# Kernel tuning notes

Measured on AMD Instinct MI355X. Metric: run time of the kernel, lower is better.

Reference implementation:

```python
import jax, jax.numpy as jnp
import numpy as np

H = 1024
B, S = 8, 2048
EPS = 1e-5


def _layernorm(x, w, b):
    m = jnp.mean(x, axis=-1, keepdims=True)
    v = jnp.mean((x - m) ** 2, axis=-1, keepdims=True)
    return (x - m) * jax.lax.rsqrt(v + EPS) * w + b


def setup_inputs() -> dict:
    key = jax.random.key(0)
    ks = jax.random.split(key, 10)
    x = jax.random.normal(ks[0], (B, S, H), dtype=jnp.float32)
    # LayerNorm params (torch default init: weight=1, bias=0)
    qn_w = jnp.ones((H,), jnp.float32)
    qn_b = jnp.zeros((H,), jnp.float32)
    kvn_w = jnp.ones((H,), jnp.float32)
    kvn_b = jnp.zeros((H,), jnp.float32)
    # q_prime/k_prime/v_prime ~ U(-0.5, 0.5)
    q_prime = jax.random.uniform(ks[1], (1, H), jnp.float32) - 0.5
    k_prime = jax.random.uniform(ks[2], (1, H), jnp.float32) - 0.5
    v_prime = jax.random.uniform(ks[3], (1, H), jnp.float32) - 0.5
    # Linear params, torch-style fan_in init
    lim = 1.0 / np.sqrt(H)
    qW = jax.random.uniform(ks[4], (H, H), jnp.float32, -lim, lim)
    qb = jax.random.uniform(ks[5], (H,), jnp.float32, -lim, lim)
    v1W = jax.random.uniform(ks[6], (H, H), jnp.float32, -lim, lim)
    v1b = jax.random.uniform(ks[7], (H,), jnp.float32, -lim, lim)
    v2W = jax.random.uniform(ks[8], (H, H), jnp.float32, -lim, lim)
    v2b = jax.random.uniform(ks[9], (H,), jnp.float32, -lim, lim)
    return {"x": x, "qn_w": qn_w, "qn_b": qn_b, "kvn_w": kvn_w, "kvn_b": kvn_b,
            "q_prime": q_prime, "k_prime": k_prime, "v_prime": v_prime,
            "qW": qW, "qb": qb, "v1W": v1W, "v1b": v1b, "v2W": v2W, "v2b": v2b}


def reference(x, qn_w, qn_b, kvn_w, kvn_b, q_prime, k_prime, v_prime,
              qW, qb, v1W, v1b, v2W, v2b):
    divisor = jnp.sqrt(jnp.float32(x.shape[-1]))
    xqn = _layernorm(x, qn_w, qn_b)            # [B,S,H]
    xkvn = _layernorm(x, kvn_w, kvn_b)         # [B,S,H]
    kr = xkvn * jax.nn.sigmoid(k_prime)        # [B,S,H]
    qr = (xqn @ qW.T + qb) * jax.nn.sigmoid(q_prime)  # [B,S,H]
    vp = jax.nn.sigmoid(v_prime)               # [1,H]
    gate = jax.nn.sigmoid(vp @ v1W.T + v1b) * jnp.tanh(vp @ v2W.T + v2b)  # [1,H]
    vr = xkvn * gate                           # [B,S,H]
    scores = jnp.einsum('bsh,bth->bst', qr, kr) / divisor  # [B,S,S]
    b, s, t = scores.shape
    # global softmax over flattened seq x seq matrix
    attn = jax.nn.softmax(scores.reshape(b, s * t), axis=-1).reshape(b, s, t)
    attended = jnp.einsum('bst,bth->bsh', attn, vr)
    return attended + xqn
```

## Files before the change

kernel.cpp:

```cpp
#include <hip/hip_runtime.h>
#include <stdint.h>


#define DEVI __device__ __forceinline__

typedef __bf16 bf16x8 __attribute__((ext_vector_type(8)));
typedef float  f32x4  __attribute__((ext_vector_type(4)));

typedef __attribute__((address_space(3))) uint32_t lds_u32_t;
typedef __attribute__((address_space(1))) uint32_t glb_u32_t;

DEVI uint16_t f2bf(float f) {
  union { float f; uint32_t u; } v; v.f = f;
  uint32_t r = (v.u + 0x7fffu + ((v.u >> 16) & 1u)) >> 16;
  return (uint16_t)r;
}
DEVI float bf2f(uint16_t b) {
  union { uint32_t u; float f; } v; v.u = ((uint32_t)b) << 16;
  return v.f;
}
DEVI float sigm(float x) { return 1.0f / (1.0f + __expf(-x)); }

DEVI void gl_lds16(const void* g, const void* lds_base) {
  __builtin_amdgcn_global_load_lds((glb_u32_t*)(uintptr_t)g,
                                   (lds_u32_t*)(uint32_t)(uintptr_t)lds_base,
                                   16, 0, 0);
}

DEVI void gemm_tile(const uint16_t* __restrict__ A, int lda,
                    const uint16_t* __restrict__ B, int ldb,
                    int K, uint16_t* sA, uint16_t* sB, f32x4 acc[4][4])
{
  const int tid  = threadIdx.x;
  const int lane = tid & 63;
  const int w    = tid >> 6;
  const int wr   = (w >> 1) * 64;
  const int wc   = (w & 1) * 64;
  const int r0   = tid >> 3;
  const int c0   = (((tid & 7) ^ (r0 & 7)) * 8);
  const int m16  = lane & 15;
  const int quad = lane >> 4;

  for (int kt = 0; kt < K; kt += 64) {
    __syncthreads();
#pragma unroll
    for (int p = 0; p < 4; p++) {
      gl_lds16(A + (size_t)(p * 32 + r0) * lda + (kt + c0), sA + (p * 32 + w * 8) * 64);
      gl_lds16(B + (size_t)(p * 32 + r0) * ldb + (kt + c0), sB + (p * 32 + w * 8) * 64);
    }
    __syncthreads();
#pragma unroll
    for (int s = 0; s < 2; s++) {
      bf16x8 af[4], bfv[4];
#pragma unroll
      for (int i = 0; i < 4; i++) {
        const int chA = ((s * 4 + quad) ^ (m16 & 7)) * 8;
        af[i]  = *(const bf16x8*)(sA + (wr + i * 16 + m16) * 64 + chA);
        bfv[i] = *(const bf16x8*)(sB + (wc + i * 16 + m16) * 64 + chA);
      }
#pragma unroll
      for (int mi = 0; mi < 4; mi++)
#pragma unroll
        for (int ni = 0; ni < 4; ni++)
          acc[mi][ni] = __builtin_amdgcn_mfma_f32_16x16x32_bf16(af[mi], bfv[ni], acc[mi][ni], 0, 0, 0);
    }
  }
}

__global__ void gate_kernel(const float* __restrict__ v_prime,
                            const float* __restrict__ v1W, const float* __restrict__ v1b,
                            const float* __restrict__ v2W, const float* __restrict__ v2b,
                            const float* __restrict__ k_prime,
                            float* __restrict__ gate2)
{
  const int tid = threadIdx.x, lane = tid & 63, w = tid >> 6;
  const int j = blockIdx.x * 4 + w;
  float d1 = 0.f, d2 = 0.f;
  for (int it = 0; it < 16; it++) {
    int i = it * 64 + lane;
    float vp = sigm(v_prime[i]);
    d1 += vp * v1W[(size_t)j * 1024 + i];
    d2 += vp * v2W[(size_t)j * 1024 + i];
  }
  for (int off = 32; off; off >>= 1) { d1 += __shfl_xor(d1, off); d2 += __shfl_xor(d2, off); }
  if (lane == 0)
    gate2[j] = sigm(d1 + v1b[j]) * tanhf(d2 + v2b[j]) / sigm(k_prime[j]);
}

__global__ void cvt_kernel(const float* __restrict__ src, uint16_t* __restrict__ dst)
{
  size_t i = ((size_t)blockIdx.x * 256 + threadIdx.x) * 4;
  float4 v = *(const float4*)(src + i);
  *(ushort4*)(dst + i) = make_ushort4(f2bf(v.x), f2bf(v.y), f2bf(v.z), f2bf(v.w));
}

__global__ __launch_bounds__(256) void ln_kernel(
    const float* __restrict__ x,
    const float* __restrict__ qn_w, const float* __restrict__ qn_b,
    const float* __restrict__ kvn_w, const float* __restrict__ kvn_b,
    const float* __restrict__ k_prime,
    uint16_t* __restrict__ xqn_bf, uint16_t* __restrict__ kr,
    float* __restrict__ krowsq)
{
  const int lane = threadIdx.x & 63, w = threadIdx.x >> 6;
  const int row = blockIdx.x * 4 + w;
  const float4* xr = (const float4*)(x + (size_t)row * 1024);
  float4 v[4];
  float s = 0.f, sq = 0.f;
#pragma unroll
  for (int i = 0; i < 4; i++) {
    v[i] = xr[i * 64 + lane];
    s  += v[i].x + v[i].y + v[i].z + v[i].w;
    sq += v[i].x * v[i].x + v[i].y * v[i].y + v[i].z * v[i].z + v[i].w * v[i].w;
  }
  for (int off = 32; off; off >>= 1) { s += __shfl_xor(s, off); sq += __shfl_xor(sq, off); }
  const float mean = s * (1.f / 1024.f);
  const float rstd = rsqrtf(sq * (1.f / 1024.f) - mean * mean + 1e-5f);

  float ksq = 0.f;
  const size_t o4 = (size_t)row * 256;
#pragma unroll
  for (int i = 0; i < 4; i++) {
    const int idx = i * 64 + lane;
    float4 qw = ((const float4*)qn_w)[idx],  qb4 = ((const float4*)qn_b)[idx];
    float4 kw = ((const float4*)kvn_w)[idx], kb4 = ((const float4*)kvn_b)[idx];
    float4 kp = ((const float4*)k_prime)[idx];
    float xn0 = (v[i].x - mean) * rstd, xn1 = (v[i].y - mean) * rstd;
    float xn2 = (v[i].z - mean) * rstd, xn3 = (v[i].w - mean) * rstd;
    float xq0 = xn0 * qw.x + qb4.x, xq1 = xn1 * qw.y + qb4.y;
    float xq2 = xn2 * qw.z + qb4.z, xq3 = xn3 * qw.w + qb4.w;
    float xk0 = xn0 * kw.x + kb4.x, xk1 = xn1 * kw.y + kb4.y;
    float xk2 = xn2 * kw.z + kb4.z, xk3 = xn3 * kw.w + kb4.w;
    float k0 = xk0 * sigm(kp.x), k1 = xk1 * sigm(kp.y);
    float k2 = xk2 * sigm(kp.z), k3 = xk3 * sigm(kp.w);
    ksq += k0 * k0 + k1 * k1 + k2 * k2 + k3 * k3;
    ((ushort4*)xqn_bf)[o4 + idx] = make_ushort4(f2bf(xq0), f2bf(xq1), f2bf(xq2), f2bf(xq3));
    ((ushort4*)kr)[o4 + idx] = make_ushort4(f2bf(k0), f2bf(k1), f2bf(k2), f2bf(k3));
  }
  for (int off = 32; off; off >>= 1) ksq += __shfl_xor(ksq, off);
  if (lane == 0) krowsq[row] = ksq;
}

__global__ __launch_bounds__(256) void qr_gemm_kernel(
    const uint16_t* __restrict__ xqn_bf, const uint16_t* __restrict__ qWbf,
    const float* __restrict__ qb, const float* __restrict__ q_prime,
    uint16_t* __restrict__ qr, float* __restrict__ qnormsq)
{
  __shared__ uint16_t sA[128 * 64], sB[128 * 64];
  f32x4 acc[4][4];
#pragma unroll
  for (int i = 0; i < 4; i++)
#pragma unroll
    for (int j = 0; j < 4; j++) acc[i][j] = (f32x4)0.0f;

  const int rowBase = blockIdx.y * 128, colBase = blockIdx.x * 128;
  gemm_tile(xqn_bf + (size_t)rowBase * 1024, 1024,
            qWbf + (size_t)colBase * 1024, 1024, 1024, sA, sB, acc);

  const int lane = threadIdx.x & 63, w = threadIdx.x >> 6;
  const int wr = (w >> 1) * 64, wc = (w & 1) * 64;
  float rsq[4][4] = {};
#pragma unroll
  for (int ni = 0; ni < 4; ni++) {
    int gc = colBase + wc + ni * 16 + (lane & 15);
    float scale = sigm(q_prime[gc]);
    float bias = qb[gc];
#pragma unroll
    for (int mi = 0; mi < 4; mi++)
#pragma unroll
      for (int r = 0; r < 4; r++) {
        int gr = rowBase + wr + mi * 16 + (lane >> 4) * 4 + r;
        float val = (acc[mi][ni][r] + bias) * scale;
        qr[(size_t)gr * 1024 + gc] = f2bf(val);
        rsq[mi][r] += val * val;
      }
  }
#pragma unroll
  for (int mi = 0; mi < 4; mi++)
#pragma unroll
    for (int r = 0; r < 4; r++) {
      float t = rsq[mi][r];
      t += __shfl_xor(t, 1); t += __shfl_xor(t, 2);
      t += __shfl_xor(t, 4); t += __shfl_xor(t, 8);
      rsq[mi][r] = t;
    }
  if ((lane & 15) == 0) {
#pragma unroll
    for (int mi = 0; mi < 4; mi++)
#pragma unroll
      for (int r = 0; r < 4; r++)
        atomicAdd(&qnormsq[rowBase + wr + mi * 16 + (lane >> 4) * 4 + r], rsq[mi][r]);
  }
}

__global__ void bound_kernel(const float* __restrict__ qnormsq,
                             const float* __restrict__ krowsq, float* __restrict__ MZ)
{
  const int b = blockIdx.x, tid = threadIdx.x, lane = tid & 63, w = tid >> 6;
  float mq = 0.f, mk = 0.f;
  for (int i = tid; i < 2048; i += 256) {
    mq = fmaxf(mq, qnormsq[b * 2048 + i]);
    mk = fmaxf(mk, krowsq[b * 2048 + i]);
  }
  for (int off = 32; off; off >>= 1) {
    mq = fmaxf(mq, __shfl_xor(mq, off));
    mk = fmaxf(mk, __shfl_xor(mk, off));
  }
  __shared__ float rm[4], rk[4];
  if (lane == 0) { rm[w] = mq; rk[w] = mk; }
  __syncthreads();
  if (tid == 0) {
    float qmax = fmaxf(fmaxf(rm[0], rm[1]), fmaxf(rm[2], rm[3]));
    float kmax = fmaxf(fmaxf(rk[0], rk[1]), fmaxf(rk[2], rk[3]));
    MZ[b] = sqrtf(qmax * kmax) * 0.03125f;
  }
}

__global__ void transpose_kernel(const uint16_t* __restrict__ kr,
                                 const float* __restrict__ gate2,
                                 uint16_t* __restrict__ vrt)
{
  __shared__ uint16_t t[64 * 72];
  const int b = blockIdx.z;
  const int t0 = blockIdx.x * 64, h0 = blockIdx.y * 64;
  const uint16_t* src = kr + (size_t)b * 2048 * 1024;
#pragma unroll
  for (int p = 0; p < 2; p++) {
    int flat = p * 256 + threadIdx.x;
    int r = flat >> 3, c = (flat & 7) * 8;
    *(uint4*)(&t[r * 72 + c]) = *(const uint4*)(src + (size_t)(t0 + r) * 1024 + h0 + c);
  }
  __syncthreads();
  uint16_t* dst = vrt + (size_t)b * 1024 * 2048;
#pragma unroll
  for (int p = 0; p < 2; p++) {
    int flat = p * 256 + threadIdx.x;
    int oh = flat >> 3, oc = (flat & 7) * 8;
    const float g = gate2[h0 + oh];
    union { uint16_t e[8]; uint4 v; } u;
#pragma unroll
    for (int j = 0; j < 8; j++) u.e[j] = f2bf(bf2f(t[(oc + j) * 72 + oh]) * g);
    *(uint4*)(dst + (size_t)(h0 + oh) * 2048 + t0 + oc) = u.v;
  }
}

__global__ __launch_bounds__(256) void scores_kernel(
    const uint16_t* __restrict__ qr, const uint16_t* __restrict__ kr,
    const float* __restrict__ MZ,
    uint16_t* __restrict__ scores, float* __restrict__ blockZ)
{
  __shared__ uint16_t sA[128 * 64], sB[128 * 64];
  __shared__ float redz[4];
  const int lid = blockIdx.x;
  const int b = lid >> 8, c = (lid >> 4) & 15, r = lid & 15;
  f32x4 acc[4][4];
#pragma unroll
  for (int i = 0; i < 4; i++)
#pragma unroll
    for (int j = 0; j < 4; j++) acc[i][j] = (f32x4)0.0f;

  const uint16_t* A = qr + (size_t)b * 2048 * 1024 + (size_t)r * 128 * 1024;
  const uint16_t* B = kr + (size_t)b * 2048 * 1024 + (size_t)c * 128 * 1024;
  gemm_tile(A, 1024, B, 1024, 1024, sA, sB, acc);

  const float Mhat = MZ[b];
  const int lane = threadIdx.x & 63, w = threadIdx.x >> 6;
  const int wr = (w >> 1) * 64, wc = (w & 1) * 64;
  uint16_t* S = scores + ((size_t)b << 22);
  const int rb = r * 128 + wr, cb = c * 128 + wc;

  float zt = 0.f;
#pragma unroll
  for (int mi = 0; mi < 4; mi++)
#pragma unroll
    for (int ni = 0; ni < 4; ni++)
#pragma unroll
      for (int rr = 0; rr < 4; rr++) {
        float p = __expf(acc[mi][ni][rr] * 0.03125f - Mhat);
        zt += p;
        S[(size_t)(rb + mi * 16 + (lane >> 4) * 4 + rr) * 2048 + (cb + ni * 16 + (lane & 15))] = f2bf(p);
      }
  for (int off = 32; off; off >>= 1) zt += __shfl_xor(zt, off);
  if (lane == 0) redz[w] = zt;
  __syncthreads();
  if (threadIdx.x == 0) blockZ[lid] = redz[0] + redz[1] + redz[2] + redz[3];
}

__global__ void zreduce_kernel(const float* __restrict__ blockZ, float* __restrict__ MZ)
{
  const int b = blockIdx.x, tid = threadIdx.x, lane = tid & 63, w = tid >> 6;
  float z = blockZ[b * 256 + tid];
  for (int off = 32; off; off >>= 1) z += __shfl_xor(z, off);
  __shared__ float rz[4];
  if (lane == 0) rz[w] = z;
  __syncthreads();
  if (tid == 0) MZ[8 + b] = rz[0] + rz[1] + rz[2] + rz[3];
}

__global__ __launch_bounds__(256) void pv_gemm_kernel(
    const uint16_t* __restrict__ P, const uint16_t* __restrict__ vrt,
    const float* __restrict__ MZ, const uint16_t* __restrict__ xqn_bf,
    float* __restrict__ out)
{
  __shared__ uint16_t sA[128 * 64], sB[128 * 64];
  const int lid = blockIdx.x;
  const int b = lid >> 7, c = (lid >> 4) & 7, r = lid & 15;
  f32x4 acc[4][4];
#pragma unroll
  for (int i = 0; i < 4; i++)
#pragma unroll
    for (int j = 0; j < 4; j++) acc[i][j] = (f32x4)0.0f;

  const uint16_t* A = P + ((size_t)b << 22) + (size_t)r * 128 * 2048;
  const uint16_t* B = vrt + (size_t)b * 1024 * 2048 + (size_t)c * 128 * 2048;
  gemm_tile(A, 2048, B, 2048, 2048, sA, sB, acc);

  const float invZ = 1.0f / MZ[8 + b];
  const int lane = threadIdx.x & 63, w = threadIdx.x >> 6;
  const int wr = (w >> 1) * 64, wc = (w & 1) * 64;
  const int rb = r * 128 + wr, cb = c * 128 + wc;
#pragma unroll
  for (int mi = 0; mi < 4; mi++)
#pragma unroll
    for (int ni = 0; ni < 4; ni++)
#pragma unroll
      for (int rr = 0; rr < 4; rr++) {
        int gr = rb + mi * 16 + (lane >> 4) * 4 + rr;
        int gc = cb + ni * 16 + (lane & 15);
        size_t o = ((size_t)b * 2048 + gr) * 1024 + gc;
        out[o] = acc[mi][ni][rr] * invZ + bf2f(xqn_bf[o]);
      }
}

extern "C" void kernel_launch(void* const* d_in, const int* in_sizes, int n_in,
                              void* d_out, int out_size, void* d_ws, size_t ws_size,
                              hipStream_t stream) {
  const float* x       = (const float*)d_in[0];
  const float* qn_w    = (const float*)d_in[1];
  const float* qn_b    = (const float*)d_in[2];
  const float* kvn_w   = (const float*)d_in[3];
  const float* kvn_b   = (const float*)d_in[4];
  const float* q_prime = (const float*)d_in[5];
  const float* k_prime = (const float*)d_in[6];
  const float* v_prime = (const float*)d_in[7];
  const float* qW      = (const float*)d_in[8];
  const float* qb      = (const float*)d_in[9];
  const float* v1W     = (const float*)d_in[10];
  const float* v1b     = (const float*)d_in[11];
  const float* v2W     = (const float*)d_in[12];
  const float* v2b     = (const float*)d_in[13];
  float* out = (float*)d_out;

  const size_t BS = 16384, H = 1024;
  char* ws = (char*)d_ws;
  size_t off = 0;
  auto alloc = [&](size_t bytes) -> char* {
    char* p = ws + off;
    off = (off + bytes + 255) & ~(size_t)255;
    return p;
  };
  float*    gate2   = (float*)alloc(H * 4);
  float*    MZ      = (float*)alloc(16 * 4);
  float*    blockZ  = (float*)alloc(2048 * 4);
  float*    qnormsq = (float*)alloc(16384 * 4);
  float*    krowsq  = (float*)alloc(16384 * 4);
  uint16_t* qWbf    = (uint16_t*)alloc(H * H * 2);
  uint16_t* xqn_bf  = (uint16_t*)alloc(BS * H * 2);
  uint16_t* kr      = (uint16_t*)alloc(BS * H * 2);
  uint16_t* scores  = (uint16_t*)alloc(BS * H * 2 * 2);
  uint16_t* vrt     = (uint16_t*)alloc(BS * H * 2);
  uint16_t* qr      = (uint16_t*)alloc(BS * H * 2);

  hipMemsetAsync(qnormsq, 0, 16384 * 4, stream);
  gate_kernel<<<256, 256, 0, stream>>>(v_prime, v1W, v1b, v2W, v2b, k_prime, gate2);
  cvt_kernel<<<1024, 256, 0, stream>>>(qW, qWbf);
  ln_kernel<<<4096, 256, 0, stream>>>(x, qn_w, qn_b, kvn_w, kvn_b, k_prime,
                                      xqn_bf, kr, krowsq);
  qr_gemm_kernel<<<dim3(8, 128), 256, 0, stream>>>(xqn_bf, qWbf, qb, q_prime, qr, qnormsq);
  transpose_kernel<<<dim3(32, 16, 8), 256, 0, stream>>>(kr, gate2, vrt);
  bound_kernel<<<8, 256, 0, stream>>>(qnormsq, krowsq, MZ);
  scores_kernel<<<2048, 256, 0, stream>>>(qr, kr, MZ, scores, blockZ);
  zreduce_kernel<<<8, 256, 0, stream>>>(blockZ, MZ);
  pv_gemm_kernel<<<1024, 256, 0, stream>>>(scores, vrt, MZ, xqn_bf, out);
}
```

Measured before the change: 395.8 us.

## Store softmax probabilities and gated values in FP8 and run PV GEMM with FP8 MFMA

The attention probabilities and the transposed gated V are now written as e4m3 FP8 instead of bf16, and the PV GEMM uses a new FP8 tile routine with 16x16x32 fp8 MFMA and 128-wide K tiles. This halves the scores and V traffic and doubles the MFMA rate for the largest GEMM. The max bound is shifted by 4 so the probabilities use more of the FP8 range. It adds a software FP8 conversion and costs precision in the output.

```diff
diff --git a/kernel.cpp b/kernel.cpp
--- a/kernel.cpp
+++ b/kernel.cpp
@@ -20,6 +20,25 @@
   return v.f;
 }
 DEVI float sigm(float x) { return 1.0f / (1.0f + __expf(-x)); }
+
+DEVI uint8_t f2e4m3(float f) {
+  union { float f; uint32_t u; } v; v.f = f;
+  uint32_t s = (v.u >> 24) & 0x80;
+  uint32_t a = v.u & 0x7fffffffu;
+  if (a >= 0x43e00000u) return s | 0x7e;
+  if (a < 0x3c800000u) {
+    float sc = __builtin_fabsf(f) * 512.0f;
+    int m = (int)(sc + 0.5f);
+    return s | (m > 7 ? 7 : m);
+  }
+  uint32_t mant = a & 0x7fffffu;
+  uint32_t exp  = a >> 23;
+  uint32_t r = mant + 0x7ffffu + ((mant >> 20) & 1u);
+  if (r & 0x800000u) { exp++; r = 0; }
+  uint32_t e8 = exp - 120u;
+  if (e8 >= 16u) return s | 0x7e;
+  return s | (e8 << 3) | ((r >> 20) & 7u);
+}
 
 DEVI void gl_lds16(const void* g, const void* lds_base) {
   __builtin_amdgcn_global_load_lds((glb_u32_t*)(uintptr_t)g,
@@ -63,6 +82,47 @@
 #pragma unroll
         for (int ni = 0; ni < 4; ni++)
           acc[mi][ni] = __builtin_amdgcn_mfma_f32_16x16x32_bf16(af[mi], bfv[ni], acc[mi][ni], 0, 0, 0);
+    }
+  }
+}
+
+DEVI void gemm_tile_f8(const uint8_t* __restrict__ A, int lda,
+                       const uint8_t* __restrict__ B, int ldb,
+                       int K, uint8_t* sA, uint8_t* sB, f32x4 acc[4][4])
+{
+  const int tid  = threadIdx.x;
+  const int lane = tid & 63;
+  const int w    = tid >> 6;
+  const int wr   = (w >> 1) * 64;
+  const int wc   = (w & 1) * 64;
+  const int r0   = tid >> 3;
+  const int c0   = (((tid & 7) ^ (r0 & 7)) * 16);
+  const int m16  = lane & 15;
+  const int quad = lane >> 4;
+  const int halfq = quad >> 1, oddq = (quad & 1) * 8, rlow = m16 & 7;
+
+  for (int kt = 0; kt < K; kt += 128) {
+    __syncthreads();
+#pragma unroll
+    for (int p = 0; p < 4; p++) {
+      gl_lds16(A + (size_t)(p * 32 + r0) * lda + (kt + c0), sA + (p * 32 + w * 8) * 128);
+      gl_lds16(B + (size_t)(p * 32 + r0) * ldb + (kt + c0), sB + (p * 32 + w * 8) * 128);
+    }
+    __syncthreads();
+#pragma unroll
+    for (int s = 0; s < 4; s++) {
+      long af[4], bfv[4];
+      const int pc = (((s * 2 + halfq) ^ rlow) * 16) + oddq;
+#pragma unroll
+      for (int i = 0; i < 4; i++) {
+        af[i]  = *(const long*)(sA + (wr + i * 16 + m16) * 128 + pc);
+        bfv[i] = *(const long*)(sB + (wc + i * 16 + m16) * 128 + pc);
+      }
+#pragma unroll
+      for (int mi = 0; mi < 4; mi++)
+#pragma unroll
+        for (int ni = 0; ni < 4; ni++)
+          acc[mi][ni] = __builtin_amdgcn_mfma_f32_16x16x32_fp8_fp8(af[mi], bfv[ni], acc[mi][ni], 0, 0, 0);
     }
   }
 }
@@ -212,13 +272,13 @@
   if (tid == 0) {
     float qmax = fmaxf(fmaxf(rm[0], rm[1]), fmaxf(rm[2], rm[3]));
     float kmax = fmaxf(fmaxf(rk[0], rk[1]), fmaxf(rk[2], rk[3]));
-    MZ[b] = sqrtf(qmax * kmax) * 0.03125f;
+    MZ[b] = sqrtf(qmax * kmax) * 0.03125f - 4.0f;
   }
 }
 
 __global__ void transpose_kernel(const uint16_t* __restrict__ kr,
                                  const float* __restrict__ gate2,
-                                 uint16_t* __restrict__ vrt)
+                                 uint8_t* __restrict__ vrt)
 {
   __shared__ uint16_t t[64 * 72];
   const int b = blockIdx.z;
@@ -231,23 +291,23 @@
     *(uint4*)(&t[r * 72 + c]) = *(const uint4*)(src + (size_t)(t0 + r) * 1024 + h0 + c);
   }
   __syncthreads();
-  uint16_t* dst = vrt + (size_t)b * 1024 * 2048;
+  uint8_t* dst = vrt + (size_t)b * 1024 * 2048;
 #pragma unroll
   for (int p = 0; p < 2; p++) {
     int flat = p * 256 + threadIdx.x;
     int oh = flat >> 3, oc = (flat & 7) * 8;
     const float g = gate2[h0 + oh];
-    union { uint16_t e[8]; uint4 v; } u;
-#pragma unroll
-    for (int j = 0; j < 8; j++) u.e[j] = f2bf(bf2f(t[(oc + j) * 72 + oh]) * g);
-    *(uint4*)(dst + (size_t)(h0 + oh) * 2048 + t0 + oc) = u.v;
+    union { uint8_t e[8]; unsigned long v; } u;
+#pragma unroll
+    for (int j = 0; j < 8; j++) u.e[j] = f2e4m3(bf2f(t[(oc + j) * 72 + oh]) * g);
+    *(unsigned long*)(dst + (size_t)(h0 + oh) * 2048 + t0 + oc) = u.v;
   }
 }
 
 __global__ __launch_bounds__(256) void scores_kernel(
     const uint16_t* __restrict__ qr, const uint16_t* __restrict__ kr,
     const float* __restrict__ MZ,
-    uint16_t* __restrict__ scores, float* __restrict__ blockZ)
+    uint8_t* __restrict__ scores, float* __restrict__ blockZ)
 {
   __shared__ uint16_t sA[128 * 64], sB[128 * 64];
   __shared__ float redz[4];
@@ -266,7 +326,7 @@
   const float Mhat = MZ[b];
   const int lane = threadIdx.x & 63, w = threadIdx.x >> 6;
   const int wr = (w >> 1) * 64, wc = (w & 1) * 64;
-  uint16_t* S = scores + ((size_t)b << 22);
+  uint8_t* S = scores + ((size_t)b << 22);
   const int rb = r * 128 + wr, cb = c * 128 + wc;
 
   float zt = 0.f;
@@ -278,7 +338,7 @@
       for (int rr = 0; rr < 4; rr++) {
         float p = __expf(acc[mi][ni][rr] * 0.03125f - Mhat);
         zt += p;
-        S[(size_t)(rb + mi * 16 + (lane >> 4) * 4 + rr) * 2048 + (cb + ni * 16 + (lane & 15))] = f2bf(p);
+        S[(size_t)(rb + mi * 16 + (lane >> 4) * 4 + rr) * 2048 + (cb + ni * 16 + (lane & 15))] = f2e4m3(p);
       }
   for (int off = 32; off; off >>= 1) zt += __shfl_xor(zt, off);
   if (lane == 0) redz[w] = zt;
@@ -298,11 +358,11 @@
 }
 
 __global__ __launch_bounds__(256) void pv_gemm_kernel(
-    const uint16_t* __restrict__ P, const uint16_t* __restrict__ vrt,
+    const uint8_t* __restrict__ P, const uint8_t* __restrict__ vrt,
     const float* __restrict__ MZ, const uint16_t* __restrict__ xqn_bf,
     float* __restrict__ out)
 {
-  __shared__ uint16_t sA[128 * 64], sB[128 * 64];
+  __shared__ uint8_t sA[128 * 128], sB[128 * 128];
   const int lid = blockIdx.x;
   const int b = lid >> 7, c = (lid >> 4) & 7, r = lid & 15;
   f32x4 acc[4][4];
@@ -311,9 +371,9 @@
 #pragma unroll
     for (int j = 0; j < 4; j++) acc[i][j] = (f32x4)0.0f;
 
-  const uint16_t* A = P + ((size_t)b << 22) + (size_t)r * 128 * 2048;
-  const uint16_t* B = vrt + (size_t)b * 1024 * 2048 + (size_t)c * 128 * 2048;
-  gemm_tile(A, 2048, B, 2048, 2048, sA, sB, acc);
+  const uint8_t* A = P + ((size_t)b << 22) + (size_t)r * 128 * 2048;
+  const uint8_t* B = vrt + (size_t)b * 1024 * 2048 + (size_t)c * 128 * 2048;
+  gemm_tile_f8(A, 2048, B, 2048, 2048, sA, sB, acc);
 
   const float invZ = 1.0f / MZ[8 + b];
   const int lane = threadIdx.x & 63, w = threadIdx.x >> 6;
@@ -367,8 +427,8 @@
   uint16_t* qWbf    = (uint16_t*)alloc(H * H * 2);
   uint16_t* xqn_bf  = (uint16_t*)alloc(BS * H * 2);
   uint16_t* kr      = (uint16_t*)alloc(BS * H * 2);
-  uint16_t* scores  = (uint16_t*)alloc(BS * H * 2 * 2);
-  uint16_t* vrt     = (uint16_t*)alloc(BS * H * 2);
+  uint8_t*  scores  = (uint8_t*)alloc(BS * H * 2);
+  uint8_t*  vrt     = (uint8_t*)alloc(BS * H);
   uint16_t* qr      = (uint16_t*)alloc(BS * H * 2);
 
   hipMemsetAsync(qnormsq, 0, 16384 * 4, stream);
```

After: 399.2 us. Within noise of the previous version (+0.9%).
